# Kernel optimization log

Hardware: AMD Instinct MI355X
Metric: run time of the kernel (lower is better)

Reference implementation:

```python
import jax, jax.numpy as jnp
import numpy as np

N, E, G = 100000, 400000, 2000
D = 128            # dim_node
DE = 128 + 300     # dim_edge after RBF concat
NC = 300           # RBF centers
CUT_LO, CUT_HI = 0.0, 30.0
N_CONV = 3


def setup_inputs() -> dict:
    key = jax.random.key(0)
    ks = jax.random.split(key, 32)
    inp = {}
    inp['Z'] = jax.random.randint(ks[0], (N,), 0, 20)
    inp['edge_type'] = jax.random.randint(ks[1], (E,), 0, 400)
    inp['dist'] = jax.random.uniform(ks[2], (E,), dtype=jnp.float32) * CUT_HI
    inp['src'] = jax.random.randint(ks[3], (E,), 0, N)
    inp['dst'] = jax.random.randint(ks[4], (E,), 0, N)
    inp['graph_ids'] = jnp.sort(jax.random.randint(ks[5], (N,), 0, G))
    s = 0.05
    inp['node_emb'] = jax.random.normal(ks[6], (20, D), jnp.float32) * s
    inp['edge_emb'] = jax.random.normal(ks[7], (400, D), jnp.float32) * s
    # per-conv-layer weights, stacked over layer dim
    inp['Wn1'] = jax.random.normal(ks[8], (N_CONV, D, D), jnp.float32) * s
    inp['bn1'] = jnp.zeros((N_CONV, D), jnp.float32)
    inp['Wn2'] = jax.random.normal(ks[9], (N_CONV, D, D), jnp.float32) * s
    inp['bn2'] = jnp.zeros((N_CONV, D), jnp.float32)
    inp['We1'] = jax.random.normal(ks[10], (N_CONV, DE, DE), jnp.float32) * s
    inp['be1'] = jnp.zeros((N_CONV, DE), jnp.float32)
    inp['We2'] = jax.random.normal(ks[11], (N_CONV, D, DE), jnp.float32) * s
    inp['be2'] = jnp.zeros((N_CONV, D), jnp.float32)
    inp['Wc'] = jax.random.normal(ks[12], (N_CONV, D, D), jnp.float32) * s
    inp['bc'] = jnp.zeros((N_CONV, D), jnp.float32)
    # read layer
    inp['Wr1'] = jax.random.normal(ks[13], (D, D), jnp.float32) * s
    inp['br1'] = jnp.zeros((D,), jnp.float32)
    inp['Wr2'] = jax.random.normal(ks[14], (1, D), jnp.float32) * s
    inp['br2'] = jnp.zeros((1,), jnp.float32)
    return inp


def _rbf(dist):
    centers = jnp.linspace(CUT_LO, CUT_HI, NC, dtype=jnp.float32)
    gap = centers[1] - centers[0]
    # [E, NC]
    return jnp.exp(-((dist[:, None] - centers[None, :]) ** 2) / gap)


def reference(Z, edge_type, dist, src, dst, graph_ids,
              node_emb, edge_emb,
              Wn1, bn1, Wn2, bn2, We1, be1, We2, be2, Wc, bc,
              Wr1, br1, Wr2, br2):
    h = node_emb[Z]                          # [N, D] node embedding
    e = edge_emb[edge_type]                  # [E, D] edge embedding
    e = jnp.concatenate([e, _rbf(dist)], axis=1)   # [E, DE]
    for i in range(N_CONV):
        hs = h[src]                          # gather src node feats [E, D]
        hn = jax.nn.relu(hs @ Wn1[i].T + bn1[i]) @ Wn2[i].T + bn2[i]   # [E, D]
        ee = jax.nn.relu(e @ We1[i].T + be1[i]) @ We2[i].T + be2[i]    # [E, D]
        m = jnp.tanh((hn * ee) @ Wc[i].T + bc[i])                      # [E, D]
        h = h + jax.ops.segment_sum(m, dst, num_segments=N)            # scatter-sum
    r = jax.nn.relu(h @ Wr1.T + br1) @ Wr2.T + br2                     # [N, 1]
    out = jax.ops.segment_sum(r, graph_ids, num_segments=G)            # [G, 1]
    return out.flatten()                                               # [G]
```

## Files before the change

### kernel.cpp

```cpp
#include <hip/hip_runtime.h>

#define NN 100000
#define En 400000
#define Gn 2000
#define GRID 2048

typedef unsigned short u16;
typedef unsigned int u32;
typedef _Float16 f16;
typedef f16 f16x8 __attribute__((ext_vector_type(8)));
typedef float f32x4 __attribute__((ext_vector_type(4)));

__device__ __forceinline__ void lds_barrier() {
  asm volatile("s_waitcnt lgkmcnt(0)\ns_barrier" ::: "memory");
}

#define MFMA16(a, b, c) __builtin_amdgcn_mfma_f32_16x16x32_f16(a, b, c, 0, 0, 0)


__global__ __launch_bounds__(256) void k_convert(const float* __restrict__ src,
                                                 f16* __restrict__ dst, int n) {
  int i = blockIdx.x * 256 + threadIdx.x;
  if (i < n) dst[i] = (f16)src[i];
}

__global__ __launch_bounds__(256) void k_pad_we2(const float* __restrict__ We2,
                                                 f16* __restrict__ dst) {
  int i = blockIdx.x * 256 + threadIdx.x;
  if (i >= 3 * 128 * 448) return;
  int l = i / 57344;
  int r = i - l * 57344;
  int row = r / 448;
  int k = r - row * 448;
  float v = (k < 428) ? We2[l * 54784 + row * 428 + k] : 0.f;
  dst[i] = (f16)v;
}

__global__ __launch_bounds__(256) void k_pad_R(const float* __restrict__ We1,
                                               f16* __restrict__ dst) {
  int i = blockIdx.x * 256 + threadIdx.x;
  if (i >= 3 * 448 * 320) return;
  int l = i / 143360;
  int r = i - l * 143360;
  int row = r / 320;
  int k = r - row * 320;
  float v = 0.f;
  if (row < 428 && k < 300) v = We1[(size_t)l * 183184 + row * 428 + 128 + k];
  dst[i] = (f16)v;
}

__global__ __launch_bounds__(256) void k_t2(const float* __restrict__ edge_emb,
                                            const float* __restrict__ We1,
                                            const float* __restrict__ be1,
                                            f16* __restrict__ T2) {
  int idx = blockIdx.x * 256 + threadIdx.x;
  if (idx >= 3 * 400 * 448) return;
  int l = idx / (400 * 448);
  int r = idx - l * (400 * 448);
  int t = r / 448;
  int j = r - t * 448;
  float s = 0.f;
  if (j < 428) {
    const float4* er = (const float4*)(edge_emb + t * 128);
    const float4* wr = (const float4*)(We1 + (size_t)l * 183184 + j * 428);
#pragma unroll
    for (int d = 0; d < 32; ++d) {
      float4 a = er[d], b = wr[d];
      s += a.x * b.x + a.y * b.y + a.z * b.z + a.w * b.w;
    }
    s += be1[l * 428 + j];
  }
  T2[idx] = (f16)s;
}

__global__ __launch_bounds__(256) void k_dtab(const f16* __restrict__ Rb,
                                              f16* __restrict__ Dtab) {
  const int tid = threadIdx.x;
  int l = blockIdx.x / (GRID + 1);
  int g = blockIdx.x - l * (GRID + 1);
  float d = (float)g * (30.f / (float)GRID);
  int kc = (int)(d * (299.f / 30.f) + 0.5f);
  int kk0 = min(max(kc - 16, 0), 268);
  __shared__ float sE[32];
  if (tid < 32) {
    float x = d - (float)(kk0 + tid) * (30.f / 299.f);
    sE[tid] = __expf(-x * x * (299.f / 30.f));
  }
  __syncthreads();
  for (int j = tid; j < 448; j += 256) {
    const f16* rr = &Rb[((size_t)l * 448 + j) * 320 + kk0];
    float s = 0.f;
#pragma unroll
    for (int k = 0; k < 32; ++k) s += sE[k] * (float)rr[k];
    Dtab[((size_t)(l * (GRID + 1) + g)) * 448 + j] = (f16)s;
  }
}

__global__ __launch_bounds__(256) void k_hinit(const int* __restrict__ Z,
                                               const float* __restrict__ node_emb,
                                               float* __restrict__ h) {
  int idx = blockIdx.x * 256 + threadIdx.x;
  int n = idx >> 5;
  int c = idx & 31;
  ((float4*)h)[idx] = ((const float4*)node_emb)[Z[n] * 32 + c];
}

__global__ __launch_bounds__(256) void k_zero_out(float* __restrict__ out) {
  int i = blockIdx.x * 256 + threadIdx.x;
  if (i < Gn) out[i] = 0.f;
}


__global__ __launch_bounds__(256) void k_zero32(u32* __restrict__ p, int n) {
  int i = blockIdx.x * 256 + threadIdx.x;
  if (i < n) p[i] = 0u;
}

__global__ __launch_bounds__(256) void k_hist(const int* __restrict__ dstv,
                                              u32* __restrict__ hist) {
  int e = blockIdx.x * 256 + threadIdx.x;
  if (e < En) atomicAdd(&hist[dstv[e]], 1u);
}

__global__ __launch_bounds__(1024) void k_scan1(const u32* __restrict__ hist,
                                                u32* __restrict__ excl,
                                                u32* __restrict__ part) {
  __shared__ u32 s[1024];
  const int t = threadIdx.x, b = blockIdx.x, i = b * 1024 + t;
  u32 v = (i < NN) ? hist[i] : 0u;
  s[t] = v;
  __syncthreads();
  u32 acc = v;
  for (int off = 1; off < 1024; off <<= 1) {
    u32 add = (t >= off) ? s[t - off] : 0u;
    __syncthreads();
    acc += add;
    s[t] = acc;
    __syncthreads();
  }
  if (i < NN) excl[i] = acc - v;
  if (t == 1023) part[b] = acc;
}

__global__ __launch_bounds__(128) void k_scan2(u32* __restrict__ part, int n) {
  __shared__ u32 s[128];
  const int t = threadIdx.x;
  u32 v = (t < n) ? part[t] : 0u;
  s[t] = v;
  __syncthreads();
  u32 acc = v;
  for (int off = 1; off < 128; off <<= 1) {
    u32 add = (t >= off) ? s[t - off] : 0u;
    __syncthreads();
    acc += add;
    s[t] = acc;
    __syncthreads();
  }
  if (t < n) part[t] = acc - v;
}

__global__ __launch_bounds__(1024) void k_scan3(const u32* __restrict__ excl,
                                                const u32* __restrict__ part,
                                                u32* __restrict__ cursor) {
  int i = blockIdx.x * 1024 + threadIdx.x;
  if (i < NN) cursor[i] = excl[i] + part[blockIdx.x];
}

__global__ __launch_bounds__(256) void k_scatter(const int* __restrict__ etype,
                                                 const float* __restrict__ dist,
                                                 const int* __restrict__ srcv,
                                                 const int* __restrict__ dstv,
                                                 u32* __restrict__ cursor,
                                                 int4* __restrict__ epack,
                                                 int* __restrict__ edst) {
  int e = blockIdx.x * 256 + threadIdx.x;
  if (e >= En) return;
  int d = dstv[e];
  int pos = (int)atomicAdd(&cursor[d], 1u);
  float fi = dist[e] * ((float)GRID / 30.f);
  int ix = (int)fi;
  epack[pos] = make_int4(srcv[e], etype[e] * 448, ix * 448,
                         __float_as_int(fi - (float)ix));
  edst[pos] = d;
}


__global__ __launch_bounds__(256) void k_node(const float* __restrict__ h,
                                              const f16* __restrict__ W1,
                                              const float* __restrict__ b1,
                                              const f16* __restrict__ W2,
                                              const float* __restrict__ b2,
                                              f16* __restrict__ n2) {
  __shared__ __align__(16) f16 sH[64 * 136];
  __shared__ __align__(16) f16 sT[64 * 136];
  const int tid = threadIdx.x;
  const int nbase = blockIdx.x * 64;
  for (int i = tid; i < 64 * 128; i += 256) {
    int e = i >> 7, d = i & 127;
    int node = nbase + e;
    float v = (node < NN) ? h[(size_t)node * 128 + d] : 0.f;
    sH[e * 136 + d] = (f16)v;
  }
  lds_barrier();
  const int lane = tid & 63, wave = tid >> 6;
  const int q = lane >> 4, ln = lane & 15;
  const int nb = wave * 32;

  f32x4 acc[4][2];
#pragma unroll
  for (int m = 0; m < 4; ++m)
#pragma unroll
    for (int n = 0; n < 2; ++n) acc[m][n] = 0.f;
#pragma unroll
  for (int k0 = 0; k0 < 128; k0 += 32) {
    f16x8 a[4];
#pragma unroll
    for (int m = 0; m < 4; ++m)
      a[m] = *(const f16x8*)&sH[(m * 16 + ln) * 136 + k0 + q * 8];
#pragma unroll
    for (int n = 0; n < 2; ++n) {
      f16x8 b = *(const f16x8*)&W1[(nb + n * 16 + ln) * 128 + k0 + q * 8];
#pragma unroll
      for (int m = 0; m < 4; ++m) acc[m][n] = MFMA16(a[m], b, acc[m][n]);
    }
  }
#pragma unroll
  for (int n = 0; n < 2; ++n) {
    int col = nb + n * 16 + ln;
    float bb = b1[col];
#pragma unroll
    for (int m = 0; m < 4; ++m)
#pragma unroll
      for (int r = 0; r < 4; ++r) {
        int row = m * 16 + q * 4 + r;
        sT[row * 136 + col] = (f16)fmaxf(acc[m][n][r] + bb, 0.f);
      }
  }
  lds_barrier();

  f32x4 acc2[4][2];
#pragma unroll
  for (int m = 0; m < 4; ++m)
#pragma unroll
    for (int n = 0; n < 2; ++n) acc2[m][n] = 0.f;
#pragma unroll
  for (int k0 = 0; k0 < 128; k0 += 32) {
    f16x8 a[4];
#pragma unroll
    for (int m = 0; m < 4; ++m)
      a[m] = *(const f16x8*)&sT[(m * 16 + ln) * 136 + k0 + q * 8];
#pragma unroll
    for (int n = 0; n < 2; ++n) {
      f16x8 b = *(const f16x8*)&W2[(nb + n * 16 + ln) * 128 + k0 + q * 8];
#pragma unroll
      for (int m = 0; m < 4; ++m) acc2[m][n] = MFMA16(a[m], b, acc2[m][n]);
    }
  }
#pragma unroll
  for (int n = 0; n < 2; ++n) {
    int col = nb + n * 16 + ln;
    float bb = b2[col];
#pragma unroll
    for (int m = 0; m < 4; ++m)
#pragma unroll
      for (int r = 0; r < 4; ++r) {
        int row = m * 16 + q * 4 + r;
        int node = nbase + row;
        if (node < NN) n2[(size_t)node * 128 + col] = (f16)(acc2[m][n][r] + bb);
      }
  }
}


__global__ __launch_bounds__(256, 4) void k_edge(
    const int4* __restrict__ epack, const int* __restrict__ edst,
    const f16* __restrict__ T2, const f16* __restrict__ Dtab,
    const f16* __restrict__ We2b, const float* __restrict__ be2,
    const f16* __restrict__ Wcb, const float* __restrict__ bc,
    const f16* __restrict__ n2, float* __restrict__ h) {
  __shared__ __align__(16) f16 sC[2][64 * 136];
  __shared__ int sSrc[64], sDst[64], sT2o[64], sIdx[64];
  __shared__ float sFrac[64];

  const int tid = threadIdx.x;
  const int e0 = blockIdx.x * 64;
  if (tid < 64) {
    int4 p = epack[e0 + tid];
    sSrc[tid] = p.x;
    sT2o[tid] = p.y;
    sIdx[tid] = p.z;
    sFrac[tid] = __int_as_float(p.w);
    sDst[tid] = edst[e0 + tid];
  }
  lds_barrier();

  const int lane = tid & 63, wave = tid >> 6;
  const int q = lane >> 4, ln = lane & 15;
  const int nb = wave * 32;

  f32x4 acc[4][2];
#pragma unroll
  for (int m = 0; m < 4; ++m)
#pragma unroll
    for (int n = 0; n < 2; ++n) acc[m][n] = 0.f;

  auto lerp_relu = [](f16x8 lo, f16x8 hi, f16x8 t2, f16 fr) -> f16x8 {
    f16x8 v = t2 + lo + (hi - lo) * fr;
    f16x8 z = {};
    return __builtin_elementwise_max(v, z);
  };

  auto prefetch128 = [&](int k0, f16x8* plo, f16x8* phi, f16x8* pt2, f16* pfr) {
    const int cg = tid & 15, eb = tid >> 4;
    const int col = k0 + cg * 8;
#pragma unroll
    for (int i = 0; i < 4; ++i) {
      int e = eb + i * 16;
      int off = sIdx[e] + col;
      plo[i] = *(const f16x8*)&Dtab[off];
      phi[i] = *(const f16x8*)&Dtab[off + 448];
      pt2[i] = *(const f16x8*)&T2[sT2o[e] + col];
      pfr[i] = (f16)sFrac[e];
    }
  };
  auto store128 = [&](f16* buf, const f16x8* plo, const f16x8* phi,
                      const f16x8* pt2, const f16* pfr) {
    const int cg = tid & 15, eb = tid >> 4;
#pragma unroll
    for (int i = 0; i < 4; ++i) {
      int e = eb + i * 16;
      *(f16x8*)&buf[e * 136 + cg * 8] = lerp_relu(plo[i], phi[i], pt2[i], pfr[i]);
    }
  };
  auto prefetch64 = [&](f16x8* plo, f16x8* phi, f16x8* pt2, f16* pfr) {
    const int cg = tid & 7, eb = tid >> 3;
    const int col = 384 + cg * 8;
#pragma unroll
    for (int i = 0; i < 2; ++i) {
      int e = eb + i * 32;
      int off = sIdx[e] + col;
      plo[i] = *(const f16x8*)&Dtab[off];
      phi[i] = *(const f16x8*)&Dtab[off + 448];
      pt2[i] = *(const f16x8*)&T2[sT2o[e] + col];
      pfr[i] = (f16)sFrac[e];
    }
  };
  auto store64 = [&](f16* buf, const f16x8* plo, const f16x8* phi,
                     const f16x8* pt2, const f16* pfr) {
    const int cg = tid & 7, eb = tid >> 3;
#pragma unroll
    for (int i = 0; i < 2; ++i) {
      int e = eb + i * 32;
      *(f16x8*)&buf[e * 136 + cg * 8] = lerp_relu(plo[i], phi[i], pt2[i], pfr[i]);
    }
  };
  auto mfma_chunk = [&](const f16* buf, int k0, int nk) {
    for (int kk = 0; kk < nk; ++kk) {
      f16x8 a[4];
#pragma unroll
      for (int m = 0; m < 4; ++m)
        a[m] = *(const f16x8*)&buf[(m * 16 + ln) * 136 + kk * 32 + q * 8];
#pragma unroll
      for (int n = 0; n < 2; ++n) {
        f16x8 b = *(const f16x8*)&We2b[(nb + n * 16 + ln) * 448 + k0 + kk * 32 + q * 8];
#pragma unroll
        for (int m = 0; m < 4; ++m) acc[m][n] = MFMA16(a[m], b, acc[m][n]);
      }
    }
  };

  {
    f16x8 plo[4], phi[4], pt2[4]; f16 pfr[4];
    prefetch128(0, plo, phi, pt2, pfr);
    store128(sC[0], plo, phi, pt2, pfr);
  }
  lds_barrier();
  {
    f16x8 plo[4], phi[4], pt2[4]; f16 pfr[4];
    prefetch128(128, plo, phi, pt2, pfr);
    mfma_chunk(sC[0], 0, 4);
    store128(sC[1], plo, phi, pt2, pfr);
  }
  lds_barrier();
  {
    f16x8 plo[4], phi[4], pt2[4]; f16 pfr[4];
    prefetch128(256, plo, phi, pt2, pfr);
    mfma_chunk(sC[1], 128, 4);
    store128(sC[0], plo, phi, pt2, pfr);
  }
  lds_barrier();
  f16x8 nrows[4];
  {
    f16x8 plo[2], phi[2], pt2[2]; f16 pfr[2];
    prefetch64(plo, phi, pt2, pfr);
#pragma unroll
    for (int i = 0; i < 4; ++i) {
      int u = tid + 256 * i;
      int e = u >> 4, cg = u & 15;
      nrows[i] = *(const f16x8*)&n2[(size_t)sSrc[e] * 128 + cg * 8];
    }
    mfma_chunk(sC[0], 256, 4);
    store64(sC[1], plo, phi, pt2, pfr);
  }
  lds_barrier();

  f16* sN = sC[0];
#pragma unroll
  for (int i = 0; i < 4; ++i) {
    int u = tid + 256 * i;
    int e = u >> 4, cg = u & 15;
    *(f16x8*)&sN[e * 136 + cg * 8] = nrows[i];
  }
  mfma_chunk(sC[1], 384, 2);
  lds_barrier();

  f16* sP = sC[1];
  {
    float be2v[2] = {be2[nb + ln], be2[nb + 16 + ln]};
#pragma unroll
    for (int n = 0; n < 2; ++n) {
      int col = nb + n * 16 + ln;
#pragma unroll
      for (int m = 0; m < 4; ++m)
#pragma unroll
        for (int r = 0; r < 4; ++r) {
          int row = m * 16 + q * 4 + r;
          float ee = acc[m][n][r] + be2v[n];
          float v = ee * (float)sN[row * 136 + col];
          sP[row * 136 + col] = (f16)v;
        }
    }
  }
  lds_barrier();

  {
    f32x4 acc2[4][2];
#pragma unroll
    for (int m = 0; m < 4; ++m)
#pragma unroll
      for (int n = 0; n < 2; ++n) acc2[m][n] = 0.f;
#pragma unroll
    for (int k0 = 0; k0 < 128; k0 += 32) {
      f16x8 a[4];
#pragma unroll
      for (int m = 0; m < 4; ++m)
        a[m] = *(const f16x8*)&sP[(m * 16 + ln) * 136 + k0 + q * 8];
#pragma unroll
      for (int n = 0; n < 2; ++n) {
        f16x8 b = *(const f16x8*)&Wcb[(nb + n * 16 + ln) * 128 + k0 + q * 8];
#pragma unroll
        for (int m = 0; m < 4; ++m) acc2[m][n] = MFMA16(a[m], b, acc2[m][n]);
      }
    }
    float bcv[2] = {bc[nb + ln], bc[nb + 16 + ln]};
#pragma unroll
    for (int m = 0; m < 4; ++m) {
      int d[4];
#pragma unroll
      for (int r = 0; r < 4; ++r) d[r] = sDst[m * 16 + q * 4 + r];
#pragma unroll
      for (int n = 0; n < 2; ++n) {
        int col = nb + n * 16 + ln;
        float t[4];
#pragma unroll
        for (int r = 0; r < 4; ++r) {
          float x = acc2[m][n][r] + bcv[n];
          x = fminf(2.f, fmaxf(-2.f, x));
          float x2 = x * x;
          t[r] = x * (15.f + x2) * __builtin_amdgcn_rcpf(15.f + 6.f * x2);
        }
        float s = t[0];
        int cur = d[0];
#pragma unroll
        for (int r = 1; r < 4; ++r) {
          if (d[r] == cur) {
            s += t[r];
          } else {
            unsafeAtomicAdd(&h[(size_t)cur * 128 + col], s);
            cur = d[r];
            s = t[r];
          }
        }
        unsafeAtomicAdd(&h[(size_t)cur * 128 + col], s);
      }
    }
  }
}


__global__ __launch_bounds__(256) void k_read(const float* __restrict__ h,
                                              const float* __restrict__ Wr1,
                                              const float* __restrict__ br1,
                                              const float* __restrict__ Wr2,
                                              const float* __restrict__ br2,
                                              const int* __restrict__ gid,
                                              float* __restrict__ out) {
  __shared__ __align__(16) f16 sH[64 * 136];
  __shared__ __align__(16) f16 sW[128 * 136];
  __shared__ float sR4[4][64];
  const int tid = threadIdx.x;
  const int nbase = blockIdx.x * 64;
  for (int i = tid; i < 64 * 128; i += 256) {
    int e = i >> 7, d = i & 127;
    int node = nbase + e;
    float v = (node < NN) ? h[(size_t)node * 128 + d] : 0.f;
    sH[e * 136 + d] = (f16)v;
  }
  for (int i = tid; i < 128 * 128; i += 256) {
    int rr = i >> 7, d = i & 127;
    sW[rr * 136 + d] = (f16)Wr1[i];
  }
  lds_barrier();
  const int lane = tid & 63, wave = tid >> 6;
  const int q = lane >> 4, ln = lane & 15;
  const int nb = wave * 32;

  f32x4 acc[4][2];
#pragma unroll
  for (int m = 0; m < 4; ++m)
#pragma unroll
    for (int n = 0; n < 2; ++n) acc[m][n] = 0.f;
#pragma unroll
  for (int k0 = 0; k0 < 128; k0 += 32) {
    f16x8 a[4];
#pragma unroll
    for (int m = 0; m < 4; ++m)
      a[m] = *(const f16x8*)&sH[(m * 16 + ln) * 136 + k0 + q * 8];
#pragma unroll
    for (int n = 0; n < 2; ++n) {
      f16x8 b = *(const f16x8*)&sW[(nb + n * 16 + ln) * 136 + k0 + q * 8];
#pragma unroll
      for (int m = 0; m < 4; ++m) acc[m][n] = MFMA16(a[m], b, acc[m][n]);
    }
  }
#pragma unroll
  for (int m = 0; m < 4; ++m)
#pragma unroll
    for (int r = 0; r < 4; ++r) {
      float t = 0.f;
#pragma unroll
      for (int n = 0; n < 2; ++n) {
        int col = nb + n * 16 + ln;
        t += fmaxf(acc[m][n][r] + br1[col], 0.f) * Wr2[col];
      }
      t += __shfl_xor(t, 1);
      t += __shfl_xor(t, 2);
      t += __shfl_xor(t, 4);
      t += __shfl_xor(t, 8);
      if (ln == 0) sR4[wave][m * 16 + q * 4 + r] = t;
    }
  lds_barrier();
  if (tid < 64) {
    int node = nbase + tid;
    if (node < NN) {
      float s = sR4[0][tid] + sR4[1][tid] + sR4[2][tid] + sR4[3][tid] + br2[0];
      unsafeAtomicAdd(&out[gid[node]], s);
    }
  }
}


extern "C" void kernel_launch(void* const* d_in, const int* in_sizes, int n_in,
                              void* d_out, int out_size, void* d_ws, size_t ws_size,
                              hipStream_t stream) {
  const int* Z = (const int*)d_in[0];
  const int* etype = (const int*)d_in[1];
  const float* dist = (const float*)d_in[2];
  const int* src = (const int*)d_in[3];
  const int* dst = (const int*)d_in[4];
  const int* gid = (const int*)d_in[5];
  const float* node_emb = (const float*)d_in[6];
  const float* edge_emb = (const float*)d_in[7];
  const float* Wn1 = (const float*)d_in[8];
  const float* bn1 = (const float*)d_in[9];
  const float* Wn2 = (const float*)d_in[10];
  const float* bn2 = (const float*)d_in[11];
  const float* We1 = (const float*)d_in[12];
  const float* be1 = (const float*)d_in[13];
  const float* We2 = (const float*)d_in[14];
  const float* be2 = (const float*)d_in[15];
  const float* Wc = (const float*)d_in[16];
  const float* bc = (const float*)d_in[17];
  const float* Wr1 = (const float*)d_in[18];
  const float* br1 = (const float*)d_in[19];
  const float* Wr2 = (const float*)d_in[20];
  const float* br2 = (const float*)d_in[21];
  float* out = (float*)d_out;

  char* ws = (char*)d_ws;
  float* h = (float*)(ws);
  f16* n2 = (f16*)(ws + 51200000);
  f16* Rb = (f16*)(ws + 76800000);
  f16* We2b = (f16*)(ws + 77660160);
  f16* Wcb = (f16*)(ws + 78004224);
  f16* Wn1b = (f16*)(ws + 78102528);
  f16* Wn2b = (f16*)(ws + 78200832);
  f16* T2 = (f16*)(ws + 78299136);
  f16* Dtab = (f16*)(ws + 79374336);
  int4* epack = (int4*)(ws + 84882048);
  int* edst = (int*)(ws + 91282048);
  u32* hist = (u32*)(ws + 92882048);
  u32* cursor = (u32*)(ws + 93282048);
  u32* excl = (u32*)(ws + 93682048);
  u32* part = (u32*)(ws + 94082048);

  k_zero32<<<391, 256, 0, stream>>>(hist, NN);
  k_hist<<<1563, 256, 0, stream>>>(dst, hist);
  k_scan1<<<98, 1024, 0, stream>>>(hist, excl, part);
  k_scan2<<<1, 128, 0, stream>>>(part, 98);
  k_scan3<<<98, 1024, 0, stream>>>(excl, part, cursor);
  k_scatter<<<1563, 256, 0, stream>>>(etype, dist, src, dst, cursor, epack, edst);

  k_convert<<<192, 256, 0, stream>>>(Wn1, Wn1b, 49152);
  k_convert<<<192, 256, 0, stream>>>(Wn2, Wn2b, 49152);
  k_convert<<<192, 256, 0, stream>>>(Wc, Wcb, 49152);
  k_pad_we2<<<672, 256, 0, stream>>>(We2, We2b);
  k_pad_R<<<1680, 256, 0, stream>>>(We1, Rb);
  k_t2<<<2100, 256, 0, stream>>>(edge_emb, We1, be1, T2);
  k_dtab<<<3 * (GRID + 1), 256, 0, stream>>>(Rb, Dtab);
  k_hinit<<<12500, 256, 0, stream>>>(Z, node_emb, h);
  k_zero_out<<<8, 256, 0, stream>>>(out);

  for (int l = 0; l < 3; ++l) {
    k_node<<<1563, 256, 0, stream>>>(h, Wn1b + l * 16384, bn1 + l * 128,
                                     Wn2b + l * 16384, bn2 + l * 128, n2);
    k_edge<<<6250, 256, 0, stream>>>(epack, edst,
                                     T2 + l * 179200, Dtab + (size_t)l * (GRID + 1) * 448,
                                     We2b + l * 57344, be2 + l * 128,
                                     Wcb + l * 16384, bc + l * 128, n2, h);
  }
  k_read<<<1563, 256, 0, stream>>>(h, Wr1, br1, Wr2, br2, gid, out);
}
```

Baseline: 979.1 us.

## Process two edge tiles per block with cross-tile prefetch; merge prep kernels

The edge kernel now handles 128 edges per block as two 64-edge tiles. It prefetches the first chunk of the second tile's gathered Dtab and T2 data while the first tile does its output GEMM and scatter, so the pipeline fill is hidden. Separately, the weight convert and pad kernels are merged into one launch, the zero-out is folded into the h-init kernel, and k_t2 is restructured to stage We1 rows in LDS. These changes cut launch count and redundant global reads, at the cost of more register pressure in the edge kernel and half as many blocks.

```diff
diff --git a/kernel.cpp b/kernel.cpp
--- a/kernel.cpp
+++ b/kernel.cpp
@@ -18,59 +18,82 @@
 #define MFMA16(a, b, c) __builtin_amdgcn_mfma_f32_16x16x32_f16(a, b, c, 0, 0, 0)
 
 
-__global__ __launch_bounds__(256) void k_convert(const float* __restrict__ src,
-                                                 f16* __restrict__ dst, int n) {
+__global__ __launch_bounds__(256) void k_prepw(
+    const float* __restrict__ Wn1, const float* __restrict__ Wn2,
+    const float* __restrict__ Wc, const float* __restrict__ We2,
+    const float* __restrict__ We1,
+    f16* __restrict__ Wn1b, f16* __restrict__ Wn2b, f16* __restrict__ Wcb,
+    f16* __restrict__ We2b, f16* __restrict__ Rb) {
   int i = blockIdx.x * 256 + threadIdx.x;
-  if (i < n) dst[i] = (f16)src[i];
-}
-
-__global__ __launch_bounds__(256) void k_pad_we2(const float* __restrict__ We2,
-                                                 f16* __restrict__ dst) {
-  int i = blockIdx.x * 256 + threadIdx.x;
-  if (i >= 3 * 128 * 448) return;
-  int l = i / 57344;
-  int r = i - l * 57344;
-  int row = r / 448;
-  int k = r - row * 448;
-  float v = (k < 428) ? We2[l * 54784 + row * 428 + k] : 0.f;
-  dst[i] = (f16)v;
-}
-
-__global__ __launch_bounds__(256) void k_pad_R(const float* __restrict__ We1,
-                                               f16* __restrict__ dst) {
-  int i = blockIdx.x * 256 + threadIdx.x;
-  if (i >= 3 * 448 * 320) return;
-  int l = i / 143360;
-  int r = i - l * 143360;
-  int row = r / 320;
-  int k = r - row * 320;
-  float v = 0.f;
-  if (row < 428 && k < 300) v = We1[(size_t)l * 183184 + row * 428 + 128 + k];
-  dst[i] = (f16)v;
-}
+  if (i < 49152) {
+    Wn1b[i] = (f16)Wn1[i];
+  } else if (i < 98304) {
+    int j = i - 49152;
+    Wn2b[j] = (f16)Wn2[j];
+  } else if (i < 147456) {
+    int j = i - 98304;
+    Wcb[j] = (f16)Wc[j];
+  } else if (i < 319488) {
+    int j = i - 147456;
+    int l = j / 57344;
+    int r = j - l * 57344;
+    int row = r / 448;
+    int k = r - row * 448;
+    float v = (k < 428) ? We2[l * 54784 + row * 428 + k] : 0.f;
+    We2b[j] = (f16)v;
+  } else if (i < 749568) {
+    int j = i - 319488;
+    int l = j / 143360;
+    int r = j - l * 143360;
+    int row = r / 320;
+    int k = r - row * 320;
+    float v = 0.f;
+    if (row < 428 && k < 300) v = We1[(size_t)l * 183184 + row * 428 + 128 + k];
+    Rb[j] = (f16)v;
+  }
+}
+
 
 __global__ __launch_bounds__(256) void k_t2(const float* __restrict__ edge_emb,
                                             const float* __restrict__ We1,
                                             const float* __restrict__ be1,
                                             f16* __restrict__ T2) {
-  int idx = blockIdx.x * 256 + threadIdx.x;
-  if (idx >= 3 * 400 * 448) return;
-  int l = idx / (400 * 448);
-  int r = idx - l * (400 * 448);
-  int t = r / 448;
-  int j = r - t * 448;
-  float s = 0.f;
-  if (j < 428) {
+  __shared__ __align__(16) float sWe[64][32 * 4];
+  __shared__ float sB[64];
+  const int tid = threadIdx.x;
+  const int l = blockIdx.x / 28;
+  const int rb = blockIdx.x - l * 28;
+  const int jb = rb >> 2;
+  const int tc = rb & 3;
+  const int j0 = jb * 64;
+  for (int idx = tid; idx < 64 * 32; idx += 256) {
+    int row = idx >> 5, c = idx & 31;
+    int gj = j0 + row;
+    float4 v = make_float4(0.f, 0.f, 0.f, 0.f);
+    if (gj < 428)
+      v = *(const float4*)&We1[(size_t)l * 183184 + gj * 428 + c * 4];
+    *(float4*)&sWe[row][c * 4] = v;
+  }
+  if (tid < 64) {
+    int gj = j0 + tid;
+    sB[tid] = (gj < 428) ? be1[l * 428 + gj] : 0.f;
+  }
+  lds_barrier();
+  const int jl = tid & 63, tl = tid >> 6;
+  const int gj = j0 + jl;
+  for (int it = 0; it < 25; ++it) {
+    int t = tc * 100 + it * 4 + tl;
     const float4* er = (const float4*)(edge_emb + t * 128);
-    const float4* wr = (const float4*)(We1 + (size_t)l * 183184 + j * 428);
+    float s = 0.f;
 #pragma unroll
     for (int d = 0; d < 32; ++d) {
-      float4 a = er[d], b = wr[d];
+      float4 a = er[d];
+      float4 b = *(const float4*)&sWe[jl][d * 4];
       s += a.x * b.x + a.y * b.y + a.z * b.z + a.w * b.w;
     }
-    s += be1[l * 428 + j];
-  }
-  T2[idx] = (f16)s;
+    s += sB[jl];
+    T2[l * 179200 + t * 448 + gj] = (gj < 428) ? (f16)s : (f16)0.f;
+  }
 }
 
 __global__ __launch_bounds__(256) void k_dtab(const f16* __restrict__ Rb,
@@ -98,16 +121,13 @@
 
 __global__ __launch_bounds__(256) void k_hinit(const int* __restrict__ Z,
                                                const float* __restrict__ node_emb,
-                                               float* __restrict__ h) {
+                                               float* __restrict__ h,
+                                               float* __restrict__ out) {
   int idx = blockIdx.x * 256 + threadIdx.x;
+  if (idx < Gn) out[idx] = 0.f;
   int n = idx >> 5;
   int c = idx & 31;
   ((float4*)h)[idx] = ((const float4*)node_emb)[Z[n] * 32 + c];
-}
-
-__global__ __launch_bounds__(256) void k_zero_out(float* __restrict__ out) {
-  int i = blockIdx.x * 256 + threadIdx.x;
-  if (i < Gn) out[i] = 0.f;
 }
 
 
@@ -279,12 +299,12 @@
     const f16* __restrict__ Wcb, const float* __restrict__ bc,
     const f16* __restrict__ n2, float* __restrict__ h) {
   __shared__ __align__(16) f16 sC[2][64 * 136];
-  __shared__ int sSrc[64], sDst[64], sT2o[64], sIdx[64];
-  __shared__ float sFrac[64];
+  __shared__ int sSrc[128], sDst[128], sT2o[128], sIdx[128];
+  __shared__ float sFrac[128];
 
   const int tid = threadIdx.x;
-  const int e0 = blockIdx.x * 64;
-  if (tid < 64) {
+  const int e0 = blockIdx.x * 128;
+  if (tid < 128) {
     int4 p = epack[e0 + tid];
     sSrc[tid] = p.x;
     sT2o[tid] = p.y;
@@ -298,24 +318,17 @@
   const int q = lane >> 4, ln = lane & 15;
   const int nb = wave * 32;
 
-  f32x4 acc[4][2];
-#pragma unroll
-  for (int m = 0; m < 4; ++m)
-#pragma unroll
-    for (int n = 0; n < 2; ++n) acc[m][n] = 0.f;
-
   auto lerp_relu = [](f16x8 lo, f16x8 hi, f16x8 t2, f16 fr) -> f16x8 {
     f16x8 v = t2 + lo + (hi - lo) * fr;
     f16x8 z = {};
     return __builtin_elementwise_max(v, z);
   };
-
-  auto prefetch128 = [&](int k0, f16x8* plo, f16x8* phi, f16x8* pt2, f16* pfr) {
+  auto pf128 = [&](int mb, int k0, f16x8* plo, f16x8* phi, f16x8* pt2, f16* pfr) {
     const int cg = tid & 15, eb = tid >> 4;
     const int col = k0 + cg * 8;
 #pragma unroll
     for (int i = 0; i < 4; ++i) {
-      int e = eb + i * 16;
+      int e = mb + eb + i * 16;
       int off = sIdx[e] + col;
       plo[i] = *(const f16x8*)&Dtab[off];
       phi[i] = *(const f16x8*)&Dtab[off + 448];
@@ -323,8 +336,8 @@
       pfr[i] = (f16)sFrac[e];
     }
   };
-  auto store128 = [&](f16* buf, const f16x8* plo, const f16x8* phi,
-                      const f16x8* pt2, const f16* pfr) {
+  auto st128 = [&](f16* buf, const f16x8* plo, const f16x8* phi,
+                   const f16x8* pt2, const f16* pfr) {
     const int cg = tid & 15, eb = tid >> 4;
 #pragma unroll
     for (int i = 0; i < 4; ++i) {
@@ -332,12 +345,12 @@
       *(f16x8*)&buf[e * 136 + cg * 8] = lerp_relu(plo[i], phi[i], pt2[i], pfr[i]);
     }
   };
-  auto prefetch64 = [&](f16x8* plo, f16x8* phi, f16x8* pt2, f16* pfr) {
+  auto pf64 = [&](int mb, f16x8* plo, f16x8* phi, f16x8* pt2, f16* pfr) {
     const int cg = tid & 7, eb = tid >> 3;
     const int col = 384 + cg * 8;
 #pragma unroll
     for (int i = 0; i < 2; ++i) {
-      int e = eb + i * 32;
+      int e = mb + eb + i * 32;
       int off = sIdx[e] + col;
       plo[i] = *(const f16x8*)&Dtab[off];
       phi[i] = *(const f16x8*)&Dtab[off + 448];
@@ -345,8 +358,8 @@
       pfr[i] = (f16)sFrac[e];
     }
   };
-  auto store64 = [&](f16* buf, const f16x8* plo, const f16x8* phi,
-                     const f16x8* pt2, const f16* pfr) {
+  auto st64 = [&](f16* buf, const f16x8* plo, const f16x8* phi,
+                  const f16x8* pt2, const f16* pfr) {
     const int cg = tid & 7, eb = tid >> 3;
 #pragma unroll
     for (int i = 0; i < 2; ++i) {
@@ -354,136 +367,151 @@
       *(f16x8*)&buf[e * 136 + cg * 8] = lerp_relu(plo[i], phi[i], pt2[i], pfr[i]);
     }
   };
-  auto mfma_chunk = [&](const f16* buf, int k0, int nk) {
-    for (int kk = 0; kk < nk; ++kk) {
-      f16x8 a[4];
-#pragma unroll
-      for (int m = 0; m < 4; ++m)
-        a[m] = *(const f16x8*)&buf[(m * 16 + ln) * 136 + kk * 32 + q * 8];
-#pragma unroll
-      for (int n = 0; n < 2; ++n) {
-        f16x8 b = *(const f16x8*)&We2b[(nb + n * 16 + ln) * 448 + k0 + kk * 32 + q * 8];
-#pragma unroll
-        for (int m = 0; m < 4; ++m) acc[m][n] = MFMA16(a[m], b, acc[m][n]);
-      }
-    }
-  };
-
-  {
-    f16x8 plo[4], phi[4], pt2[4]; f16 pfr[4];
-    prefetch128(0, plo, phi, pt2, pfr);
-    store128(sC[0], plo, phi, pt2, pfr);
-  }
-  lds_barrier();
-  {
-    f16x8 plo[4], phi[4], pt2[4]; f16 pfr[4];
-    prefetch128(128, plo, phi, pt2, pfr);
-    mfma_chunk(sC[0], 0, 4);
-    store128(sC[1], plo, phi, pt2, pfr);
-  }
-  lds_barrier();
-  {
-    f16x8 plo[4], phi[4], pt2[4]; f16 pfr[4];
-    prefetch128(256, plo, phi, pt2, pfr);
-    mfma_chunk(sC[1], 128, 4);
-    store128(sC[0], plo, phi, pt2, pfr);
-  }
-  lds_barrier();
-  f16x8 nrows[4];
-  {
-    f16x8 plo[2], phi[2], pt2[2]; f16 pfr[2];
-    prefetch64(plo, phi, pt2, pfr);
+
+  f16x8 PnLo[4], PnHi[4], PnT2[4];
+  f16 PnFr[4];
+
+  for (int t = 0; t < 2; ++t) {
+    const int mb = t * 64;
+    f32x4 acc[4][2];
+#pragma unroll
+    for (int m = 0; m < 4; ++m)
+#pragma unroll
+      for (int n = 0; n < 2; ++n) acc[m][n] = 0.f;
+
+    auto mfma_chunk = [&](const f16* buf, int k0, int nk) {
+      for (int kk = 0; kk < nk; ++kk) {
+        f16x8 a[4];
+#pragma unroll
+        for (int m = 0; m < 4; ++m)
+          a[m] = *(const f16x8*)&buf[(m * 16 + ln) * 136 + kk * 32 + q * 8];
+#pragma unroll
+        for (int n = 0; n < 2; ++n) {
+          f16x8 b = *(const f16x8*)&We2b[(nb + n * 16 + ln) * 448 + k0 + kk * 32 + q * 8];
+#pragma unroll
+          for (int m = 0; m < 4; ++m) acc[m][n] = MFMA16(a[m], b, acc[m][n]);
+        }
+      }
+    };
+
+    if (t == 0) {
+      f16x8 plo[4], phi[4], pt2[4]; f16 pfr[4];
+      pf128(mb, 0, plo, phi, pt2, pfr);
+      st128(sC[0], plo, phi, pt2, pfr);
+      lds_barrier();
+    }
+    {
+      f16x8 plo[4], phi[4], pt2[4]; f16 pfr[4];
+      pf128(mb, 128, plo, phi, pt2, pfr);
+      mfma_chunk(sC[0], 0, 4);
+      st128(sC[1], plo, phi, pt2, pfr);
+    }
+    lds_barrier();
+    {
+      f16x8 plo[4], phi[4], pt2[4]; f16 pfr[4];
+      pf128(mb, 256, plo, phi, pt2, pfr);
+      mfma_chunk(sC[1], 128, 4);
+      st128(sC[0], plo, phi, pt2, pfr);
+    }
+    lds_barrier();
+    f16x8 nrows[4];
+    {
+      f16x8 plo[2], phi[2], pt2[2]; f16 pfr[2];
+      pf64(mb, plo, phi, pt2, pfr);
+#pragma unroll
+      for (int i = 0; i < 4; ++i) {
+        int u = tid + 256 * i;
+        int e = u >> 4, cg = u & 15;
+        nrows[i] = *(const f16x8*)&n2[(size_t)sSrc[mb + e] * 128 + cg * 8];
+      }
+      mfma_chunk(sC[0], 256, 4);
+      st64(sC[1], plo, phi, pt2, pfr);
+    }
+    lds_barrier();
+
+    f16* sN = sC[0];
 #pragma unroll
     for (int i = 0; i < 4; ++i) {
       int u = tid + 256 * i;
       int e = u >> 4, cg = u & 15;
-      nrows[i] = *(const f16x8*)&n2[(size_t)sSrc[e] * 128 + cg * 8];
-    }
-    mfma_chunk(sC[0], 256, 4);
-    store64(sC[1], plo, phi, pt2, pfr);
-  }
-  lds_barrier();
-
-  f16* sN = sC[0];
-#pragma unroll
-  for (int i = 0; i < 4; ++i) {
-    int u = tid + 256 * i;
-    int e = u >> 4, cg = u & 15;
-    *(f16x8*)&sN[e * 136 + cg * 8] = nrows[i];
-  }
-  mfma_chunk(sC[1], 384, 2);
-  lds_barrier();
-
-  f16* sP = sC[1];
-  {
-    float be2v[2] = {be2[nb + ln], be2[nb + 16 + ln]};
-#pragma unroll
-    for (int n = 0; n < 2; ++n) {
-      int col = nb + n * 16 + ln;
-#pragma unroll
-      for (int m = 0; m < 4; ++m)
-#pragma unroll
-        for (int r = 0; r < 4; ++r) {
-          int row = m * 16 + q * 4 + r;
-          float ee = acc[m][n][r] + be2v[n];
-          float v = ee * (float)sN[row * 136 + col];
-          sP[row * 136 + col] = (f16)v;
-        }
-    }
-  }
-  lds_barrier();
-
-  {
-    f32x4 acc2[4][2];
-#pragma unroll
-    for (int m = 0; m < 4; ++m)
-#pragma unroll
-      for (int n = 0; n < 2; ++n) acc2[m][n] = 0.f;
-#pragma unroll
-    for (int k0 = 0; k0 < 128; k0 += 32) {
-      f16x8 a[4];
-#pragma unroll
-      for (int m = 0; m < 4; ++m)
-        a[m] = *(const f16x8*)&sP[(m * 16 + ln) * 136 + k0 + q * 8];
-#pragma unroll
-      for (int n = 0; n < 2; ++n) {
-        f16x8 b = *(const f16x8*)&Wcb[(nb + n * 16 + ln) * 128 + k0 + q * 8];
-#pragma unroll
-        for (int m = 0; m < 4; ++m) acc2[m][n] = MFMA16(a[m], b, acc2[m][n]);
-      }
-    }
-    float bcv[2] = {bc[nb + ln], bc[nb + 16 + ln]};
-#pragma unroll
-    for (int m = 0; m < 4; ++m) {
-      int d[4];
-#pragma unroll
-      for (int r = 0; r < 4; ++r) d[r] = sDst[m * 16 + q * 4 + r];
+      *(f16x8*)&sN[e * 136 + cg * 8] = nrows[i];
+    }
+    mfma_chunk(sC[1], 384, 2);
+    lds_barrier();
+
+    f16* sP = sC[1];
+    {
+      float be2v[2] = {be2[nb + ln], be2[nb + 16 + ln]};
 #pragma unroll
       for (int n = 0; n < 2; ++n) {
         int col = nb + n * 16 + ln;
-        float t[4];
-#pragma unroll
-        for (int r = 0; r < 4; ++r) {
-          float x = acc2[m][n][r] + bcv[n];
-          x = fminf(2.f, fmaxf(-2.f, x));
-          float x2 = x * x;
-          t[r] = x * (15.f + x2) * __builtin_amdgcn_rcpf(15.f + 6.f * x2);
+#pragma unroll
+        for (int m = 0; m < 4; ++m)
+#pragma unroll
+          for (int r = 0; r < 4; ++r) {
+            int row = m * 16 + q * 4 + r;
+            float ee = acc[m][n][r] + be2v[n];
+            sP[row * 136 + col] = (f16)(ee * (float)sN[row * 136 + col]);
+          }
+      }
+    }
+    if (t == 0) pf128(64, 0, PnLo, PnHi, PnT2, PnFr);
+    lds_barrier();
+
+    {
+      f32x4 acc2[4][2];
+#pragma unroll
+      for (int m = 0; m < 4; ++m)
+#pragma unroll
+        for (int n = 0; n < 2; ++n) acc2[m][n] = 0.f;
+#pragma unroll
+      for (int k0 = 0; k0 < 128; k0 += 32) {
+        f16x8 a[4];
+#pragma unroll
+        for (int m = 0; m < 4; ++m)
+          a[m] = *(const f16x8*)&sP[(m * 16 + ln) * 136 + k0 + q * 8];
+#pragma unroll
+        for (int n = 0; n < 2; ++n) {
+          f16x8 b = *(const f16x8*)&Wcb[(nb + n * 16 + ln) * 128 + k0 + q * 8];
+#pragma unroll
+          for (int m = 0; m < 4; ++m) acc2[m][n] = MFMA16(a[m], b, acc2[m][n]);
         }
-        float s = t[0];
-        int cur = d[0];
-#pragma unroll
-        for (int r = 1; r < 4; ++r) {
-          if (d[r] == cur) {
-            s += t[r];
-          } else {
-            unsafeAtomicAdd(&h[(size_t)cur * 128 + col], s);
-            cur = d[r];
-            s = t[r];
+      }
+      if (t == 0) st128(sC[0], PnLo, PnHi, PnT2, PnFr);
+      float bcv[2] = {bc[nb + ln], bc[nb + 16 + ln]};
+#pragma unroll
+      for (int m = 0; m < 4; ++m) {
+        int d[4];
+#pragma unroll
+        for (int r = 0; r < 4; ++r) d[r] = sDst[mb + m * 16 + q * 4 + r];
+#pragma unroll
+        for (int n = 0; n < 2; ++n) {
+          int col = nb + n * 16 + ln;
+          float tv[4];
+#pragma unroll
+          for (int r = 0; r < 4; ++r) {
+            float x = acc2[m][n][r] + bcv[n];
+            x = fminf(2.f, fmaxf(-2.f, x));
+            float x2 = x * x;
+            tv[r] = x * (15.f + x2) * __builtin_amdgcn_rcpf(15.f + 6.f * x2);
           }
+          float s = tv[0];
+          int cur = d[0];
+#pragma unroll
+          for (int r = 1; r < 4; ++r) {
+            if (d[r] == cur) {
+              s += tv[r];
+            } else {
+              unsafeAtomicAdd(&h[(size_t)cur * 128 + col], s);
+              cur = d[r];
+              s = tv[r];
+            }
+          }
+          unsafeAtomicAdd(&h[(size_t)cur * 128 + col], s);
         }
-        unsafeAtomicAdd(&h[(size_t)cur * 128 + col], s);
-      }
-    }
+      }
+    }
+    lds_barrier();
   }
 }
 
@@ -611,20 +639,16 @@
   k_scan3<<<98, 1024, 0, stream>>>(excl, part, cursor);
   k_scatter<<<1563, 256, 0, stream>>>(etype, dist, src, dst, cursor, epack, edst);
 
-  k_convert<<<192, 256, 0, stream>>>(Wn1, Wn1b, 49152);
-  k_convert<<<192, 256, 0, stream>>>(Wn2, Wn2b, 49152);
-  k_convert<<<192, 256, 0, stream>>>(Wc, Wcb, 49152);
-  k_pad_we2<<<672, 256, 0, stream>>>(We2, We2b);
-  k_pad_R<<<1680, 256, 0, stream>>>(We1, Rb);
-  k_t2<<<2100, 256, 0, stream>>>(edge_emb, We1, be1, T2);
+  k_prepw<<<2928, 256, 0, stream>>>(Wn1, Wn2, Wc, We2, We1,
+                                    Wn1b, Wn2b, Wcb, We2b, Rb);
+  k_t2<<<84, 256, 0, stream>>>(edge_emb, We1, be1, T2);
   k_dtab<<<3 * (GRID + 1), 256, 0, stream>>>(Rb, Dtab);
-  k_hinit<<<12500, 256, 0, stream>>>(Z, node_emb, h);
-  k_zero_out<<<8, 256, 0, stream>>>(out);
+  k_hinit<<<12500, 256, 0, stream>>>(Z, node_emb, h, out);
 
   for (int l = 0; l < 3; ++l) {
     k_node<<<1563, 256, 0, stream>>>(h, Wn1b + l * 16384, bn1 + l * 128,
                                      Wn2b + l * 16384, bn2 + l * 128, n2);
-    k_edge<<<6250, 256, 0, stream>>>(epack, edst,
+    k_edge<<<3125, 256, 0, stream>>>(epack, edst,
                                      T2 + l * 179200, Dtab + (size_t)l * (GRID + 1) * 448,
                                      We2b + l * 57344, be2 + l * 128,
                                      Wcb + l * 16384, bc + l * 128, n2, h);
```

Result: slower. 1.250 ms (+27.6%).
